# Performance work log

Measured on AMD Instinct MI355X. Metric: run time of the kernel, lower is better.

## Reference

```python
import jax, jax.numpy as jnp
import numpy as np

NUM_GOALS = 4
STATE_DIM = 256
HID = 256
HEAD_HID = 128
OUT = 128
BATCH = 131072
LN_EPS = 1e-5


def setup_inputs() -> dict:
    key = jax.random.key(0)
    ks = jax.random.split(key, 10)
    s = 0.02
    return {
        "x": jax.random.normal(ks[0], (BATCH, STATE_DIM + NUM_GOALS), dtype=jnp.float32),
        "W0": jax.random.normal(ks[1], (STATE_DIM, HID), dtype=jnp.float32) * s,
        "b0": jnp.zeros((HID,), dtype=jnp.float32),
        "gamma": jnp.ones((HID,), dtype=jnp.float32),
        "beta": jnp.zeros((HID,), dtype=jnp.float32),
        "W1": jax.random.normal(ks[2], (NUM_GOALS, HID, HEAD_HID), dtype=jnp.float32) * s,
        "b1": jnp.zeros((NUM_GOALS, HEAD_HID), dtype=jnp.float32),
        "W2": jax.random.normal(ks[3], (NUM_GOALS, HEAD_HID, OUT), dtype=jnp.float32) * s,
        "b2": jnp.zeros((NUM_GOALS, OUT), dtype=jnp.float32),
    }


def reference(x, W0, b0, gamma, beta, W1, b1, W2, b2):
    x = x.astype(jnp.float32)
    state = x[:, :-NUM_GOALS]          # [B, STATE_DIM]
    goal = x[:, -NUM_GOALS:]           # [B, G]
    # shared trunk: Linear -> LayerNorm -> LeakyReLU(0.1)
    h = state @ W0 + b0                # [B, HID]
    mu = jnp.mean(h, axis=-1, keepdims=True)
    var = jnp.mean((h - mu) ** 2, axis=-1, keepdims=True)
    h = (h - mu) / jnp.sqrt(var + LN_EPS) * gamma + beta
    h = jnp.where(h >= 0, h, 0.1 * h)  # LeakyReLU(0.1)
    # all heads densely (faithful to stack-then-gather original)
    t = jax.nn.relu(jnp.einsum("bd,gdh->bgh", h, W1) + b1)   # [B, G, HEAD_HID]
    all_out = jnp.einsum("bgh,gho->bgo", t, W2) + b2         # [B, G, OUT]
    goal_idx = jnp.argmax(goal, axis=1)                      # [B]
    return jnp.take_along_axis(all_out, goal_idx[:, None, None], axis=1)[:, 0, :]
```

## Files before the change

kernel.cpp:

```cpp
#include <hip/hip_runtime.h>

#define BATCH 131072
#define XDIM 260
#define SDIM 256
#define HID 256
#define HHID 128
#define ODIM 128

typedef __attribute__((ext_vector_type(8))) short short8;
typedef __attribute__((ext_vector_type(4))) short short4v;
typedef __attribute__((ext_vector_type(4))) float floatx4;
typedef __attribute__((ext_vector_type(8))) _Float16 half8;

__device__ __forceinline__ short f2h(float f) {
    union { _Float16 h; short s; } u;
    u.h = (_Float16)f;
    return u.s;
}

__global__ void prep_kernel(const float* __restrict__ W0, const float* __restrict__ W1,
                            const float* __restrict__ W2, short* __restrict__ W0F,
                            short* __restrict__ W1F, short* __restrict__ W2F,
                            int* __restrict__ cursor) {
    int i = blockIdx.x * 256 + threadIdx.x;
    if (i < 4) cursor[i] = 0;
    if (i < 65536) {
        int e = i & 7, lane = (i >> 3) & 63, kit = (i >> 9) & 7, c = (i >> 12) & 15;
        int col = c * 16 + (lane & 15);
        int k = kit * 32 + (lane >> 4) * 8 + e;
        W0F[i] = f2h(W0[k * HID + col]);
    }
    {
        int e = i & 7, lane = (i >> 3) & 63, kit = (i >> 9) & 7, c = (i >> 12) & 7, g = i >> 15;
        int col = c * 16 + (lane & 15);
        int k = kit * 32 + (lane >> 4) * 8 + e;
        W1F[i] = f2h(W1[(g * SDIM + k) * HHID + col]);
    }
    if (i < 65536) {
        int e = i & 7, lane = (i >> 3) & 63, kit = (i >> 9) & 3, c = (i >> 11) & 7, g = i >> 14;
        int col = c * 16 + (lane & 15);
        int k = kit * 32 + (lane >> 4) * 8 + e;
        W2F[i] = f2h(W2[(g * HHID + k) * ODIM + col]);
    }
}

__global__ void bucket_kernel(const float* __restrict__ x, int* __restrict__ cursor,
                              int* __restrict__ perm) {
    __shared__ int lhist[4];
    __shared__ int lbase[4];
    const int tid = threadIdx.x;
    if (tid < 4) lhist[tid] = 0;
    __syncthreads();

    const int row = blockIdx.x * 256 + tid;
    const float4 gv = *reinterpret_cast<const float4*>(x + (size_t)row * XDIM + SDIM);
    int gi = 0; float best = gv.x;
    if (gv.y > best) { best = gv.y; gi = 1; }
    if (gv.z > best) { best = gv.z; gi = 2; }
    if (gv.w > best) { best = gv.w; gi = 3; }

    const int lpos = atomicAdd(&lhist[gi], 1);
    __syncthreads();
    if (tid < 4) lbase[tid] = atomicAdd(&cursor[tid], lhist[tid]);
    __syncthreads();
    perm[gi * BATCH + lbase[gi] + lpos] = row;
}

__global__ __launch_bounds__(256, 4) void k1_gemm_ln(
        const float* __restrict__ x, const float* __restrict__ b0,
        const float* __restrict__ gamma, const float* __restrict__ beta,
        const short* __restrict__ W0F, short* __restrict__ H) {
    __shared__ __align__(16) short a_lds[64][264];
    __shared__ float psum[64][4];
    __shared__ float psq[64][4];
    __shared__ float mu_s[64];
    __shared__ float rs_s[64];

    const int tid = threadIdx.x;
    const int lane = tid & 63;
    const int w = tid >> 6;
    const int m0 = blockIdx.x * 64;

    #pragma unroll
    for (int half = 0; half < 2; ++half) {
        float4 v[8];
        #pragma unroll
        for (int c = 0; c < 8; ++c) {
            int s = (half * 8 + c) * 256 + tid;
            int row = s >> 6;
            int k4 = (s & 63) << 2;
            v[c] = *reinterpret_cast<const float4*>(x + (size_t)(m0 + row) * XDIM + k4);
        }
        __builtin_amdgcn_sched_barrier(0);
        #pragma unroll
        for (int c = 0; c < 8; ++c) {
            int s = (half * 8 + c) * 256 + tid;
            int row = s >> 6;
            int k4 = (s & 63) << 2;
            short4v sv;
            sv.x = f2h(v[c].x); sv.y = f2h(v[c].y); sv.z = f2h(v[c].z); sv.w = f2h(v[c].w);
            *reinterpret_cast<short4v*>(&a_lds[row][k4]) = sv;
        }
    }
    __syncthreads();

    const int q = lane >> 4;
    const int l15 = lane & 15;

    floatx4 acc[4][4] = {};
    const short8* B0 = reinterpret_cast<const short8*>(W0F) + (w << 11) + lane;

    #pragma unroll
    for (int kit = 0; kit < 8; ++kit) {
        half8 af[4], bf[4];
        #pragma unroll
        for (int mi = 0; mi < 4; ++mi)
            af[mi] = *reinterpret_cast<const half8*>(&a_lds[mi * 16 + l15][kit * 32 + q * 8]);
        #pragma unroll
        for (int ni = 0; ni < 4; ++ni)
            bf[ni] = *reinterpret_cast<const half8*>(&B0[(ni << 9) + (kit << 6)]);
        #pragma unroll
        for (int mi = 0; mi < 4; ++mi)
            #pragma unroll
            for (int ni = 0; ni < 4; ++ni)
                acc[mi][ni] = __builtin_amdgcn_mfma_f32_16x16x32_f16(af[mi], bf[ni], acc[mi][ni], 0, 0, 0);
    }

    float bias[4], gm[4], bt[4];
    #pragma unroll
    for (int ni = 0; ni < 4; ++ni) {
        int col = (w << 6) + ni * 16 + l15;
        bias[ni] = b0[col]; gm[ni] = gamma[col]; bt[ni] = beta[col];
    }
    #pragma unroll
    for (int mi = 0; mi < 4; ++mi) {
        #pragma unroll
        for (int r = 0; r < 4; ++r) {
            float s = 0.f, ss = 0.f;
            #pragma unroll
            for (int ni = 0; ni < 4; ++ni) {
                float v = acc[mi][ni][r] + bias[ni];
                acc[mi][ni][r] = v;
                s += v; ss += v * v;
            }
            #pragma unroll
            for (int off = 1; off < 16; off <<= 1) {
                s  += __shfl_xor(s,  off, 64);
                ss += __shfl_xor(ss, off, 64);
            }
            if (l15 == 0) {
                int row = mi * 16 + q * 4 + r;
                psum[row][w] = s;
                psq[row][w]  = ss;
            }
        }
    }
    __syncthreads();
    if (tid < 64) {
        float s  = psum[tid][0] + psum[tid][1] + psum[tid][2] + psum[tid][3];
        float ss = psq[tid][0]  + psq[tid][1]  + psq[tid][2]  + psq[tid][3];
        float mu = s * (1.f / 256.f);
        float var = ss * (1.f / 256.f) - mu * mu;
        mu_s[tid] = mu;
        rs_s[tid] = rsqrtf(var + 1e-5f);
    }
    __syncthreads();

    #pragma unroll
    for (int mi = 0; mi < 4; ++mi) {
        #pragma unroll
        for (int r = 0; r < 4; ++r) {
            int row = mi * 16 + q * 4 + r;
            float mu = mu_s[row], rs = rs_s[row];
            short* dst = H + (size_t)(m0 + row) * HID + (w << 6) + l15;
            #pragma unroll
            for (int ni = 0; ni < 4; ++ni) {
                float v = (acc[mi][ni][r] - mu) * rs * gm[ni] + bt[ni];
                v = (v >= 0.f) ? v : 0.1f * v;
                dst[ni * 16] = f2h(v);
            }
        }
    }
}

__global__ __launch_bounds__(256, 2) void k2_heads(
        const short* H, const short* __restrict__ W1F, const short* __restrict__ W2F,
        const float* __restrict__ b1, const float* __restrict__ b2,
        const int* __restrict__ cursor, const int* __restrict__ perm,
        float* out) {
    const int g = blockIdx.y;
    const int t = blockIdx.x;
    const int cnt = cursor[g];
    if (t * 64 >= cnt) return;

    __shared__ __align__(16) short a_lds[64][264];
    __shared__ __align__(16) short t_lds[64][136];
    __shared__ int rows_s[64];

    const int tid = threadIdx.x;
    const int lane = tid & 63;
    const int w = tid >> 6;
    const int* pg = perm + (size_t)g * BATCH;

    if (tid < 64) {
        int idx = t * 64 + tid;
        rows_s[tid] = pg[idx < cnt ? idx : cnt - 1];
    }
    __syncthreads();

    #pragma unroll
    for (int c = 0; c < 8; ++c) {
        int s = c * 256 + tid;
        int row = s >> 5;
        int k8 = (s & 31) << 3;
        short8 v = *reinterpret_cast<const short8*>(H + (size_t)rows_s[row] * HID + k8);
        *reinterpret_cast<short8*>(&a_lds[row][k8]) = v;
    }
    __syncthreads();

    const int q = lane >> 4;
    const int l15 = lane & 15;

    floatx4 acc1[4][2] = {};
    const short8* B1 = reinterpret_cast<const short8*>(W1F) + (g << 12) + (w << 10) + lane;
    #pragma unroll
    for (int kit = 0; kit < 8; ++kit) {
        half8 af[4], bf[2];
        #pragma unroll
        for (int mi = 0; mi < 4; ++mi)
            af[mi] = *reinterpret_cast<const half8*>(&a_lds[mi * 16 + l15][kit * 32 + q * 8]);
        #pragma unroll
        for (int ni = 0; ni < 2; ++ni)
            bf[ni] = *reinterpret_cast<const half8*>(&B1[(ni << 9) + (kit << 6)]);
        #pragma unroll
        for (int mi = 0; mi < 4; ++mi)
            #pragma unroll
            for (int ni = 0; ni < 2; ++ni)
                acc1[mi][ni] = __builtin_amdgcn_mfma_f32_16x16x32_f16(af[mi], bf[ni], acc1[mi][ni], 0, 0, 0);
    }
    #pragma unroll
    for (int ni = 0; ni < 2; ++ni) {
        int col = (w << 5) + ni * 16 + l15;
        float bb = b1[g * HHID + col];
        #pragma unroll
        for (int mi = 0; mi < 4; ++mi)
            #pragma unroll
            for (int r = 0; r < 4; ++r) {
                int row = mi * 16 + q * 4 + r;
                float v = acc1[mi][ni][r] + bb;
                t_lds[row][col] = f2h(v > 0.f ? v : 0.f);
            }
    }
    __syncthreads();

    floatx4 acc2[4][2] = {};
    const short8* B2 = reinterpret_cast<const short8*>(W2F) + (g << 11) + (w << 9) + lane;
    #pragma unroll
    for (int kit = 0; kit < 4; ++kit) {
        half8 af[4], bf[2];
        #pragma unroll
        for (int mi = 0; mi < 4; ++mi)
            af[mi] = *reinterpret_cast<const half8*>(&t_lds[mi * 16 + l15][kit * 32 + q * 8]);
        #pragma unroll
        for (int ni = 0; ni < 2; ++ni)
            bf[ni] = *reinterpret_cast<const half8*>(&B2[(ni << 8) + (kit << 6)]);
        #pragma unroll
        for (int mi = 0; mi < 4; ++mi)
            #pragma unroll
            for (int ni = 0; ni < 2; ++ni)
                acc2[mi][ni] = __builtin_amdgcn_mfma_f32_16x16x32_f16(af[mi], bf[ni], acc2[mi][ni], 0, 0, 0);
    }
    #pragma unroll
    for (int ni = 0; ni < 2; ++ni) {
        int col = (w << 5) + ni * 16 + l15;
        float bb = b2[g * ODIM + col];
        #pragma unroll
        for (int mi = 0; mi < 4; ++mi)
            #pragma unroll
            for (int r = 0; r < 4; ++r) {
                int row = mi * 16 + q * 4 + r;
                int idx = t * 64 + row;
                if (idx < cnt)
                    out[(size_t)rows_s[row] * ODIM + col] = acc2[mi][ni][r] + bb;
            }
    }
}

extern "C" void kernel_launch(void* const* d_in, const int* in_sizes, int n_in,
                              void* d_out, int out_size, void* d_ws, size_t ws_size,
                              hipStream_t stream) {
    const float* x     = (const float*)d_in[0];
    const float* W0    = (const float*)d_in[1];
    const float* b0    = (const float*)d_in[2];
    const float* gamma = (const float*)d_in[3];
    const float* beta  = (const float*)d_in[4];
    const float* W1    = (const float*)d_in[5];
    const float* b1    = (const float*)d_in[6];
    const float* W2    = (const float*)d_in[7];
    const float* b2    = (const float*)d_in[8];

    char* ws = (char*)d_ws;
    short* W0F  = (short*)(ws);
    short* W1F  = (short*)(ws + 131072);
    short* W2F  = (short*)(ws + 393216);
    int* cursor = (int*)(ws + 524288);
    int* perm   = (int*)(ws + 525312);
    short* H    = (short*)d_out;
    float* out  = (float*)d_out;

    prep_kernel<<<512, 256, 0, stream>>>(W0, W1, W2, W0F, W1F, W2F, cursor);
    bucket_kernel<<<512, 256, 0, stream>>>(x, cursor, perm);
    k1_gemm_ln<<<BATCH / 64, 256, 0, stream>>>(x, b0, gamma, beta, W0F, H);
    k2_heads<<<dim3(BATCH / 64, 4), 256, 0, stream>>>(H, W1F, W2F, b1, b2, cursor, perm, out);
}
```

Before: 111.2 us.

## Make k1 persistent with double-buffered LDS and register prefetch of next x tile

The trunk GEMM+LayerNorm kernel now launches 512 persistent blocks that each process 4 row tiles. The next tile's x rows are loaded into registers while the current tile's MFMAs run, then converted and written into a second LDS buffer. The aim is to hide global-load latency behind compute. The cost is 16 float4 prefetch registers, double the LDS, and launch bounds lowered to 2 blocks per SM, which cuts occupancy.

```diff
diff --git a/kernel.cpp b/kernel.cpp
--- a/kernel.cpp
+++ b/kernel.cpp
@@ -6,6 +6,8 @@
 #define HID 256
 #define HHID 128
 #define ODIM 128
+#define NBLK 512
+#define TILES 4
 
 typedef __attribute__((ext_vector_type(8))) short short8;
 typedef __attribute__((ext_vector_type(4))) short short4v;
@@ -66,11 +68,11 @@
     perm[gi * BATCH + lbase[gi] + lpos] = row;
 }
 
-__global__ __launch_bounds__(256, 4) void k1_gemm_ln(
+__global__ __launch_bounds__(256, 2) void k1_gemm_ln(
         const float* __restrict__ x, const float* __restrict__ b0,
         const float* __restrict__ gamma, const float* __restrict__ beta,
         const short* __restrict__ W0F, short* __restrict__ H) {
-    __shared__ __align__(16) short a_lds[64][264];
+    __shared__ __align__(16) short a_lds[2][64][264];
     __shared__ float psum[64][4];
     __shared__ float psq[64][4];
     __shared__ float mu_s[64];
@@ -79,105 +81,147 @@
     const int tid = threadIdx.x;
     const int lane = tid & 63;
     const int w = tid >> 6;
-    const int m0 = blockIdx.x * 64;
-
-    #pragma unroll
-    for (int half = 0; half < 2; ++half) {
-        float4 v[8];
-        #pragma unroll
-        for (int c = 0; c < 8; ++c) {
-            int s = (half * 8 + c) * 256 + tid;
+    const int q = lane >> 4;
+    const int l15 = lane & 15;
+
+    const short8* B0 = reinterpret_cast<const short8*>(W0F) + (w << 11) + lane;
+
+    {
+        const int m0 = blockIdx.x * 64;
+        #pragma unroll
+        for (int half = 0; half < 2; ++half) {
+            float4 v[8];
+            #pragma unroll
+            for (int c = 0; c < 8; ++c) {
+                int s = (half * 8 + c) * 256 + tid;
+                int row = s >> 6;
+                int k4 = (s & 63) << 2;
+                v[c] = *reinterpret_cast<const float4*>(x + (size_t)(m0 + row) * XDIM + k4);
+            }
+            __builtin_amdgcn_sched_barrier(0);
+            #pragma unroll
+            for (int c = 0; c < 8; ++c) {
+                int s = (half * 8 + c) * 256 + tid;
+                int row = s >> 6;
+                int k4 = (s & 63) << 2;
+                short4v sv;
+                sv.x = f2h(v[c].x); sv.y = f2h(v[c].y); sv.z = f2h(v[c].z); sv.w = f2h(v[c].w);
+                *reinterpret_cast<short4v*>(&a_lds[0][row][k4]) = sv;
+            }
+        }
+    }
+
+    float4 vp[16];
+    {
+        const int m1 = (blockIdx.x + NBLK) * 64;
+        #pragma unroll
+        for (int c = 0; c < 16; ++c) {
+            int s = c * 256 + tid;
             int row = s >> 6;
             int k4 = (s & 63) << 2;
-            v[c] = *reinterpret_cast<const float4*>(x + (size_t)(m0 + row) * XDIM + k4);
+            vp[c] = *reinterpret_cast<const float4*>(x + (size_t)(m1 + row) * XDIM + k4);
         }
         __builtin_amdgcn_sched_barrier(0);
-        #pragma unroll
-        for (int c = 0; c < 8; ++c) {
-            int s = (half * 8 + c) * 256 + tid;
-            int row = s >> 6;
-            int k4 = (s & 63) << 2;
-            short4v sv;
-            sv.x = f2h(v[c].x); sv.y = f2h(v[c].y); sv.z = f2h(v[c].z); sv.w = f2h(v[c].w);
-            *reinterpret_cast<short4v*>(&a_lds[row][k4]) = sv;
-        }
-    }
-    __syncthreads();
-
-    const int q = lane >> 4;
-    const int l15 = lane & 15;
-
-    floatx4 acc[4][4] = {};
-    const short8* B0 = reinterpret_cast<const short8*>(W0F) + (w << 11) + lane;
-
-    #pragma unroll
-    for (int kit = 0; kit < 8; ++kit) {
-        half8 af[4], bf[4];
-        #pragma unroll
-        for (int mi = 0; mi < 4; ++mi)
-            af[mi] = *reinterpret_cast<const half8*>(&a_lds[mi * 16 + l15][kit * 32 + q * 8]);
-        #pragma unroll
-        for (int ni = 0; ni < 4; ++ni)
-            bf[ni] = *reinterpret_cast<const half8*>(&B0[(ni << 9) + (kit << 6)]);
-        #pragma unroll
-        for (int mi = 0; mi < 4; ++mi)
+    }
+
+    for (int t = 0; t < TILES; ++t) {
+        const int cur = t & 1;
+        const int m0 = (blockIdx.x + t * NBLK) * 64;
+        __syncthreads();
+
+        floatx4 acc[4][4] = {};
+        #pragma unroll
+        for (int kit = 0; kit < 8; ++kit) {
+            half8 af[4], bf[4];
+            #pragma unroll
+            for (int mi = 0; mi < 4; ++mi)
+                af[mi] = *reinterpret_cast<const half8*>(&a_lds[cur][mi * 16 + l15][kit * 32 + q * 8]);
             #pragma unroll
             for (int ni = 0; ni < 4; ++ni)
-                acc[mi][ni] = __builtin_amdgcn_mfma_f32_16x16x32_f16(af[mi], bf[ni], acc[mi][ni], 0, 0, 0);
-    }
-
-    float bias[4], gm[4], bt[4];
-    #pragma unroll
-    for (int ni = 0; ni < 4; ++ni) {
-        int col = (w << 6) + ni * 16 + l15;
-        bias[ni] = b0[col]; gm[ni] = gamma[col]; bt[ni] = beta[col];
-    }
-    #pragma unroll
-    for (int mi = 0; mi < 4; ++mi) {
-        #pragma unroll
-        for (int r = 0; r < 4; ++r) {
-            float s = 0.f, ss = 0.f;
-            #pragma unroll
-            for (int ni = 0; ni < 4; ++ni) {
-                float v = acc[mi][ni][r] + bias[ni];
-                acc[mi][ni][r] = v;
-                s += v; ss += v * v;
-            }
-            #pragma unroll
-            for (int off = 1; off < 16; off <<= 1) {
-                s  += __shfl_xor(s,  off, 64);
-                ss += __shfl_xor(ss, off, 64);
-            }
-            if (l15 == 0) {
+                bf[ni] = *reinterpret_cast<const half8*>(&B0[(ni << 9) + (kit << 6)]);
+            #pragma unroll
+            for (int mi = 0; mi < 4; ++mi)
+                #pragma unroll
+                for (int ni = 0; ni < 4; ++ni)
+                    acc[mi][ni] = __builtin_amdgcn_mfma_f32_16x16x32_f16(af[mi], bf[ni], acc[mi][ni], 0, 0, 0);
+        }
+
+        if (t < TILES - 1) {
+            #pragma unroll
+            for (int c = 0; c < 16; ++c) {
+                int s = c * 256 + tid;
+                int row = s >> 6;
+                int k4 = (s & 63) << 2;
+                short4v sv;
+                sv.x = f2h(vp[c].x); sv.y = f2h(vp[c].y); sv.z = f2h(vp[c].z); sv.w = f2h(vp[c].w);
+                *reinterpret_cast<short4v*>(&a_lds[cur ^ 1][row][k4]) = sv;
+            }
+            if (t < TILES - 2) {
+                const int mn = (blockIdx.x + (t + 2) * NBLK) * 64;
+                #pragma unroll
+                for (int c = 0; c < 16; ++c) {
+                    int s = c * 256 + tid;
+                    int row = s >> 6;
+                    int k4 = (s & 63) << 2;
+                    vp[c] = *reinterpret_cast<const float4*>(x + (size_t)(mn + row) * XDIM + k4);
+                }
+                __builtin_amdgcn_sched_barrier(0);
+            }
+        }
+
+        float bias[4], gm[4], bt[4];
+        #pragma unroll
+        for (int ni = 0; ni < 4; ++ni) {
+            int col = (w << 6) + ni * 16 + l15;
+            bias[ni] = b0[col]; gm[ni] = gamma[col]; bt[ni] = beta[col];
+        }
+        #pragma unroll
+        for (int mi = 0; mi < 4; ++mi) {
+            #pragma unroll
+            for (int r = 0; r < 4; ++r) {
+                float s = 0.f, ss = 0.f;
+                #pragma unroll
+                for (int ni = 0; ni < 4; ++ni) {
+                    float v = acc[mi][ni][r] + bias[ni];
+                    acc[mi][ni][r] = v;
+                    s += v; ss += v * v;
+                }
+                #pragma unroll
+                for (int off = 1; off < 16; off <<= 1) {
+                    s  += __shfl_xor(s,  off, 64);
+                    ss += __shfl_xor(ss, off, 64);
+                }
+                if (l15 == 0) {
+                    int row = mi * 16 + q * 4 + r;
+                    psum[row][w] = s;
+                    psq[row][w]  = ss;
+                }
+            }
+        }
+        __syncthreads();
+        if (tid < 64) {
+            float s  = psum[tid][0] + psum[tid][1] + psum[tid][2] + psum[tid][3];
+            float ss = psq[tid][0]  + psq[tid][1]  + psq[tid][2]  + psq[tid][3];
+            float mu = s * (1.f / 256.f);
+            float var = ss * (1.f / 256.f) - mu * mu;
+            mu_s[tid] = mu;
+            rs_s[tid] = rsqrtf(var + 1e-5f);
+        }
+        __syncthreads();
+
+        #pragma unroll
+        for (int mi = 0; mi < 4; ++mi) {
+            #pragma unroll
+            for (int r = 0; r < 4; ++r) {
                 int row = mi * 16 + q * 4 + r;
-                psum[row][w] = s;
-                psq[row][w]  = ss;
-            }
-        }
-    }
-    __syncthreads();
-    if (tid < 64) {
-        float s  = psum[tid][0] + psum[tid][1] + psum[tid][2] + psum[tid][3];
-        float ss = psq[tid][0]  + psq[tid][1]  + psq[tid][2]  + psq[tid][3];
-        float mu = s * (1.f / 256.f);
-        float var = ss * (1.f / 256.f) - mu * mu;
-        mu_s[tid] = mu;
-        rs_s[tid] = rsqrtf(var + 1e-5f);
-    }
-    __syncthreads();
-
-    #pragma unroll
-    for (int mi = 0; mi < 4; ++mi) {
-        #pragma unroll
-        for (int r = 0; r < 4; ++r) {
-            int row = mi * 16 + q * 4 + r;
-            float mu = mu_s[row], rs = rs_s[row];
-            short* dst = H + (size_t)(m0 + row) * HID + (w << 6) + l15;
-            #pragma unroll
-            for (int ni = 0; ni < 4; ++ni) {
-                float v = (acc[mi][ni][r] - mu) * rs * gm[ni] + bt[ni];
-                v = (v >= 0.f) ? v : 0.1f * v;
-                dst[ni * 16] = f2h(v);
+                float mu = mu_s[row], rs = rs_s[row];
+                short* dst = H + (size_t)(m0 + row) * HID + (w << 6) + l15;
+                #pragma unroll
+                for (int ni = 0; ni < 4; ++ni) {
+                    float v = (acc[mi][ni][r] - mu) * rs * gm[ni] + bt[ni];
+                    v = (v >= 0.f) ? v : 0.1f * v;
+                    dst[ni * 16] = f2h(v);
+                }
             }
         }
     }
@@ -310,6 +354,6 @@
 
     prep_kernel<<<512, 256, 0, stream>>>(W0, W1, W2, W0F, W1F, W2F, cursor);
     bucket_kernel<<<512, 256, 0, stream>>>(x, cursor, perm);
-    k1_gemm_ln<<<BATCH / 64, 256, 0, stream>>>(x, b0, gamma, beta, W0F, H);
+    k1_gemm_ln<<<NBLK, 256, 0, stream>>>(x, b0, gamma, beta, W0F, H);
     k2_heads<<<dim3(BATCH / 64, 4), 256, 0, stream>>>(H, W1F, W2F, b1, b2, cursor, perm, out);
 }
```

Measured after the change: 165.4 us. 1.49x slower.

## Pre-convert x to fp16 MFMA fragment layout in a separate kernel

Applied to the files above, without the earlier changes.

Adds a kernel that converts the fp32 state part of x to fp16 and writes it into the output buffer in the exact per-lane MFMA fragment order. The trunk GEMM then loads A fragments straight from global memory instead of staging through LDS, which removes the LDS tile and a barrier and may raise occupancy. In exchange it adds a kernel launch plus an extra write and read of the fp16 activations. H is also written in place over XB, so correctness depends on each block reading only its own tile before overwriting it.

```diff
diff --git a/kernel.cpp b/kernel.cpp
--- a/kernel.cpp
+++ b/kernel.cpp
@@ -8,7 +8,6 @@
 #define ODIM 128
 
 typedef __attribute__((ext_vector_type(8))) short short8;
-typedef __attribute__((ext_vector_type(4))) short short4v;
 typedef __attribute__((ext_vector_type(4))) float floatx4;
 typedef __attribute__((ext_vector_type(8))) _Float16 half8;
 
@@ -66,11 +65,31 @@
     perm[gi * BATCH + lbase[gi] + lpos] = row;
 }
 
-__global__ __launch_bounds__(256, 4) void k1_gemm_ln(
-        const float* __restrict__ x, const float* __restrict__ b0,
+__global__ void xcvt_kernel(const float* __restrict__ x, short* __restrict__ XB) {
+    const int tid = threadIdx.x;
+    const int tile = blockIdx.x;
+    const int m0 = tile * 64;
+    short8* X8 = reinterpret_cast<short8*>(XB) + ((size_t)tile << 11);
+    #pragma unroll
+    for (int i = 0; i < 8; ++i) {
+        int s = i * 256 + tid;
+        int r = s >> 5;
+        int c = s & 31;
+        const float* xr = x + (size_t)(m0 + r) * XDIM + c * 8;
+        float4 a = *reinterpret_cast<const float4*>(xr);
+        float4 b = *reinterpret_cast<const float4*>(xr + 4);
+        short8 sv;
+        sv[0] = f2h(a.x); sv[1] = f2h(a.y); sv[2] = f2h(a.z); sv[3] = f2h(a.w);
+        sv[4] = f2h(b.x); sv[5] = f2h(b.y); sv[6] = f2h(b.z); sv[7] = f2h(b.w);
+        int kit = c >> 2, q = c & 3, mi = r >> 4, l15 = r & 15;
+        X8[(kit << 8) + (mi << 6) + (q << 4) + l15] = sv;
+    }
+}
+
+__global__ __launch_bounds__(256, 4) void k1d_gemm_ln(
+        const short* XB, const float* __restrict__ b0,
         const float* __restrict__ gamma, const float* __restrict__ beta,
-        const short* __restrict__ W0F, short* __restrict__ H) {
-    __shared__ __align__(16) short a_lds[64][264];
+        const short* __restrict__ W0F, short* H) {
     __shared__ float psum[64][4];
     __shared__ float psq[64][4];
     __shared__ float mu_s[64];
@@ -79,43 +98,21 @@
     const int tid = threadIdx.x;
     const int lane = tid & 63;
     const int w = tid >> 6;
-    const int m0 = blockIdx.x * 64;
-
-    #pragma unroll
-    for (int half = 0; half < 2; ++half) {
-        float4 v[8];
-        #pragma unroll
-        for (int c = 0; c < 8; ++c) {
-            int s = (half * 8 + c) * 256 + tid;
-            int row = s >> 6;
-            int k4 = (s & 63) << 2;
-            v[c] = *reinterpret_cast<const float4*>(x + (size_t)(m0 + row) * XDIM + k4);
-        }
-        __builtin_amdgcn_sched_barrier(0);
-        #pragma unroll
-        for (int c = 0; c < 8; ++c) {
-            int s = (half * 8 + c) * 256 + tid;
-            int row = s >> 6;
-            int k4 = (s & 63) << 2;
-            short4v sv;
-            sv.x = f2h(v[c].x); sv.y = f2h(v[c].y); sv.z = f2h(v[c].z); sv.w = f2h(v[c].w);
-            *reinterpret_cast<short4v*>(&a_lds[row][k4]) = sv;
-        }
-    }
-    __syncthreads();
-
     const int q = lane >> 4;
     const int l15 = lane & 15;
+    const int tile = blockIdx.x;
+    const int m0 = tile * 64;
+
+    const short8* A0 = reinterpret_cast<const short8*>(XB) + ((size_t)tile << 11);
+    const short8* B0 = reinterpret_cast<const short8*>(W0F) + (w << 11) + lane;
 
     floatx4 acc[4][4] = {};
-    const short8* B0 = reinterpret_cast<const short8*>(W0F) + (w << 11) + lane;
-
     #pragma unroll
     for (int kit = 0; kit < 8; ++kit) {
         half8 af[4], bf[4];
         #pragma unroll
         for (int mi = 0; mi < 4; ++mi)
-            af[mi] = *reinterpret_cast<const half8*>(&a_lds[mi * 16 + l15][kit * 32 + q * 8]);
+            af[mi] = *reinterpret_cast<const half8*>(&A0[(kit << 8) + (mi << 6) + lane]);
         #pragma unroll
         for (int ni = 0; ni < 4; ++ni)
             bf[ni] = *reinterpret_cast<const half8*>(&B0[(ni << 9) + (kit << 6)]);
@@ -305,11 +302,12 @@
     short* W2F  = (short*)(ws + 393216);
     int* cursor = (int*)(ws + 524288);
     int* perm   = (int*)(ws + 525312);
-    short* H    = (short*)d_out;
+    short* XB   = (short*)d_out;
     float* out  = (float*)d_out;
 
     prep_kernel<<<512, 256, 0, stream>>>(W0, W1, W2, W0F, W1F, W2F, cursor);
     bucket_kernel<<<512, 256, 0, stream>>>(x, cursor, perm);
-    k1_gemm_ln<<<BATCH / 64, 256, 0, stream>>>(x, b0, gamma, beta, W0F, H);
-    k2_heads<<<dim3(BATCH / 64, 4), 256, 0, stream>>>(H, W1F, W2F, b1, b2, cursor, perm, out);
-}
+    xcvt_kernel<<<BATCH / 64, 256, 0, stream>>>(x, XB);
+    k1d_gemm_ln<<<BATCH / 64, 256, 0, stream>>>(XB, b0, gamma, beta, W0F, XB);
+    k2_heads<<<dim3(BATCH / 64, 4), 256, 0, stream>>>(XB, W1F, W2F, b1, b2, cursor, perm, out);
+}
```

Result: slower. 135.1 us (+21.5%).
